# Kernel optimization log

Hardware: AMD Instinct MI355X
Metric: run time of the kernel (lower is better)

The kernel has to match this reference:

```python
import jax, jax.numpy as jnp
import numpy as np

N_NODES, N_EDGES, N_GRAPHS = 20000, 320000, 16
F_NODE, F_EDGE, F_GLOB = 64, 32, 16


def seg_mean(x, idx, num):
    # segment average; segments with zero members yield zeros
    s = jax.ops.segment_sum(x, idx, num_segments=num)
    c = jax.ops.segment_sum(jnp.ones((x.shape[0], 1), x.dtype), idx, num_segments=num)
    return s / jnp.maximum(c, 1.0)


def setup_inputs() -> dict:
    key = jax.random.key(0)
    ks = jax.random.split(key, 24)
    s = 0.05
    inp = {
        'node_feats': jax.random.normal(ks[0], (N_NODES, F_NODE), jnp.float32),
        'edge_feats': jax.random.normal(ks[1], (N_EDGES, F_EDGE), jnp.float32),
        'globals_': jax.random.normal(ks[2], (N_GRAPHS, F_GLOB), jnp.float32),
        'We1': jax.random.normal(ks[3], (256, F_EDGE), jnp.float32) * s,
        'be1': jnp.zeros((256,), jnp.float32),
        'Wn1': jax.random.normal(ks[4], (256, F_NODE), jnp.float32) * s,
        'Win1': jax.random.normal(ks[5], (256, 256), jnp.float32) * s,
        'bn1': jnp.zeros((256,), jnp.float32),
        'We2': jax.random.normal(ks[6], (128, 256), jnp.float32) * s,
        'Wg2': jax.random.normal(ks[7], (128, F_GLOB), jnp.float32) * s,
        'be2': jnp.zeros((128,), jnp.float32),
        'Wn2': jax.random.normal(ks[8], (128, 256), jnp.float32) * s,
        'Win2': jax.random.normal(ks[9], (128, 128), jnp.float32) * s,
        'Wng2': jax.random.normal(ks[10], (128, F_GLOB), jnp.float32) * s,
        'bn2': jnp.zeros((128,), jnp.float32),
        'Wgn': jax.random.normal(ks[11], (128, 128), jnp.float32) * s,
        'Wge': jax.random.normal(ks[12], (128, 128), jnp.float32) * s,
        'Wgg': jax.random.normal(ks[13], (128, F_GLOB), jnp.float32) * s,
        'bg': jnp.zeros((128,), jnp.float32),
        'receivers': jax.random.randint(ks[14], (N_EDGES,), 0, N_NODES, jnp.int32),
        'node_graph': jnp.sort(jax.random.randint(ks[15], (N_NODES,), 0, N_GRAPHS, jnp.int32)),
    }
    return inp


def reference(node_feats, edge_feats, globals_, We1, be1, Wn1, Win1, bn1,
              We2, Wg2, be2, Wn2, Win2, Wng2, bn2, Wgn, Wge, Wgg, bg,
              receivers, node_graph):
    N = node_feats.shape[0]
    B = globals_.shape[0]
    edge_graph = node_graph[receivers]  # graph id of each edge [E]

    # edge1 + relu: e -> 256
    e1 = jax.nn.relu(edge_feats @ We1.T + be1)  # [E,256]
    # node1 + relu: node + avg incoming edges -> 256
    agg1 = seg_mean(e1, receivers, N)  # [N,256]
    n1 = jax.nn.relu(node_feats @ Wn1.T + agg1 @ Win1.T + bn1)  # [N,256]
    # edge2 + relu: edge + broadcast globals -> 128
    e2 = jax.nn.relu(e1 @ We2.T + globals_[edge_graph] @ Wg2.T + be2)  # [E,128]
    # node2 + relu: node + avg incoming edges + broadcast globals -> 128
    agg2 = seg_mean(e2, receivers, N)  # [N,128]
    n2 = jax.nn.relu(n1 @ Wn2.T + agg2 @ Win2.T + globals_[node_graph] @ Wng2.T + bn2)  # [N,128]
    # global: avg nodes + avg edges per graph + globals -> output
    node_avg = seg_mean(n2, node_graph, B)  # [B,128]
    edge_avg = seg_mean(e2, edge_graph, B)  # [B,128]
    out = node_avg @ Wgn.T + edge_avg @ Wge.T + globals_ @ Wgg.T + bg  # [B,128]
    return out
```

## Files before the change

### kernel.cpp

```cpp
#include <hip/hip_runtime.h>
#include <hip/hip_bf16.h>

#define N_NODES 20000
#define N_EDGES 320000
#define NG 16

using bf16 = __hip_bfloat16;
typedef __attribute__((ext_vector_type(8))) short short8v;
typedef __attribute__((ext_vector_type(4))) short short4v;
typedef __attribute__((ext_vector_type(4))) float f32x4;

static __device__ __forceinline__ short f2bs(float f) {
  bf16 h = __float2bfloat16(f);
  union { bf16 b; short s; } u;
  u.b = h;
  return u.s;
}
static __device__ __forceinline__ float bs2f(short s) {
  union { short s; bf16 b; } u;
  u.s = s;
  return __bfloat162float(u.b);
}

__global__ __launch_bounds__(256) void k_prep(
    const float* __restrict__ globals_, const float* __restrict__ Wg2,
    const float* __restrict__ Wng2, const float* __restrict__ Wgg,
    const float* __restrict__ bg, float* __restrict__ g2e,
    float* __restrict__ g2n, float* __restrict__ gg,
    const float* __restrict__ We1, const float* __restrict__ Wn1,
    const float* __restrict__ Win1, const float* __restrict__ We2,
    const float* __restrict__ Wn2, const float* __restrict__ Win2,
    bf16* __restrict__ Wb_e1, bf16* __restrict__ Wb_n1,
    bf16* __restrict__ Wb_e2, bf16* __restrict__ Wb_n2,
    const float* __restrict__ nf, bf16* __restrict__ nfb) {
  int idx = blockIdx.x * 256 + threadIdx.x;
  if (idx < 6144) {
    int arr = idx >> 11;
    int rem = idx & 2047;
    int g = rem >> 7, c = rem & 127;
    const float* W = arr == 0 ? Wg2 : (arr == 1 ? Wng2 : Wgg);
    float acc = (arr == 2) ? bg[c] : 0.f;
#pragma unroll
    for (int k = 0; k < 16; ++k) acc += globals_[g * 16 + k] * W[c * 16 + k];
    float* o = arr == 0 ? g2e : (arr == 1 ? g2n : gg);
    o[rem] = acc;
    return;
  }
  idx -= 6144;
  if (idx < 172032) {
    int i = idx;
    float v;
    bf16* dst;
    int di;
    if (i < 8192) {
      v = We1[i]; dst = Wb_e1; di = i;
    } else if (i < 90112) {
      int j = i - 8192, r = j / 320, c = j % 320;
      v = c < 64 ? Wn1[r * 64 + c] : Win1[r * 256 + (c - 64)];
      dst = Wb_n1; di = j;
    } else if (i < 122880) {
      int j = i - 90112;
      int n = j >> 8, p = j & 255;
      int k = ((p & 15) << 4) | (p >> 4);
      v = We2[n * 256 + k];
      dst = Wb_e2; di = j;
    } else {
      int j = i - 122880, r = j / 384, c = j % 384;
      if (c < 256) {
        int k = ((c & 15) << 4) | (c >> 4);
        v = Wn2[r * 256 + k];
      } else {
        v = Win2[r * 128 + (c - 256)];
      }
      dst = Wb_n2; di = j;
    }
    dst[di] = __float2bfloat16(v);
    return;
  }
  idx -= 172032;
  if (idx < 320000) {
    int n = idx >> 4, q = idx & 15;
    float4 v = *(const float4*)(nf + (size_t)n * 64 + q * 4);
    short4v o = {f2bs(v.x), f2bs(v.y), f2bs(v.z), f2bs(v.w)};
    *(short4v*)((short*)nfb + (size_t)n * 64 + q * 4) = o;
  }
}

__global__ __launch_bounds__(256) void k_counts(
    const int* __restrict__ recv, const int* __restrict__ node_graph,
    int* __restrict__ cnt_node, int* __restrict__ node_cnt_g,
    int* __restrict__ edge_cnt_g) {
  __shared__ int le[NG], ln[NG];
  int tid = threadIdx.x;
  if (tid < NG) { le[tid] = 0; ln[tid] = 0; }
  __syncthreads();
  int idx = blockIdx.x * 256 + tid;
  if (idx < N_EDGES) {
    int r = recv[idx];
    atomicAdd(&cnt_node[r], 1);
    atomicAdd(&le[node_graph[r]], 1);
  } else if (idx < N_EDGES + N_NODES) {
    int n = idx - N_EDGES;
    atomicAdd(&ln[node_graph[n]], 1);
  }
  __syncthreads();
  if (tid < NG && le[tid]) atomicAdd(&edge_cnt_g[tid], le[tid]);
  if (tid >= NG && tid < 2 * NG && ln[tid - NG]) atomicAdd(&node_cnt_g[tid - NG], ln[tid - NG]);
}

__global__ __launch_bounds__(256) void k_scan(const int* __restrict__ cnt,
                                              int* __restrict__ offset,
                                              int* __restrict__ cursor) {
  __shared__ int wsum[4];
  __shared__ int carry_s;
  int tid = threadIdx.x, lane = tid & 63, wv = tid >> 6;
  if (tid == 0) carry_s = 0;
  __syncthreads();
  for (int base = 0; base < N_NODES; base += 1024) {
    int idx = base + tid * 4;
    int v[4];
    int s = 0;
#pragma unroll
    for (int i = 0; i < 4; ++i) {
      v[i] = (idx + i < N_NODES) ? cnt[idx + i] : 0;
      s += v[i];
    }
    int ps = s;
#pragma unroll
    for (int d = 1; d < 64; d <<= 1) {
      int t = __shfl_up(ps, d, 64);
      if (lane >= d) ps += t;
    }
    if (lane == 63) wsum[wv] = ps;
    __syncthreads();
    int wbase = carry_s;
    for (int w2 = 0; w2 < wv; ++w2) wbase += wsum[w2];
    int run = wbase + ps - s;
#pragma unroll
    for (int i = 0; i < 4; ++i) {
      if (idx + i < N_NODES) {
        offset[idx + i] = run;
        cursor[idx + i] = 0;
      }
      run += v[i];
    }
    __syncthreads();
    if (tid == 0) carry_s += wsum[0] + wsum[1] + wsum[2] + wsum[3];
    __syncthreads();
  }
  if (tid == 0) offset[N_NODES] = carry_s;
}

__global__ __launch_bounds__(256) void k_scatter(
    const int* __restrict__ recv, const int* __restrict__ offset,
    int* __restrict__ cursor, int* __restrict__ pos2edge,
    int* __restrict__ pos2node) {
  int e = blockIdx.x * 256 + threadIdx.x;
  if (e >= N_EDGES) return;
  int n = recv[e];
  int slot = atomicAdd(&cursor[n], 1);
  int pos = offset[n] + slot;
  pos2edge[pos] = e;
  pos2node[pos] = n;
}

__global__ __launch_bounds__(256, 3) void k_edge(
    const float* __restrict__ edge_feats, const bf16* __restrict__ We1b,
    const bf16* __restrict__ We2b, const float* __restrict__ be1,
    const float* __restrict__ be2, const float* __restrict__ g2e,
    const int* __restrict__ pos2edge, const int* __restrict__ pos2node,
    const int* __restrict__ node_graph, const int* __restrict__ offset,
    float* __restrict__ agg1f, float* __restrict__ agg2f) {
  __shared__ __align__(16) char wlds[16384];
  __shared__ __align__(16) short t16[64 * 264];
  __shared__ int rownode_s[64];
  __shared__ int rowgid_s[64];
  const int tid = threadIdx.x;
  const int wave = tid >> 6, lane = tid & 63;
  const int l15 = lane & 15, grp = lane >> 4;
  const int p0 = blockIdx.x * 64;
  const int base = wave * 16;

  if (tid < 64) {
    int rn = pos2node[p0 + tid];
    rownode_s[tid] = rn;
    rowgid_s[tid] = node_graph[rn];
  }
  const int n0w = tid >> 3, cgw = tid & 7;
  short8v wreg[4];
#pragma unroll
  for (int s = 0; s < 4; ++s)
    wreg[s] = *(const short8v*)((const short*)We2b + (size_t)(n0w + s * 32) * 256 + cgw * 8);
#pragma unroll
  for (int s = 0; s < 4; ++s) {
    int slot = tid + s * 256;
    int n = slot >> 2, cg = slot & 3;
    short8v w8 = *(const short8v*)((const short*)We1b + n * 32 + cg * 8);
    *(short8v*)(wlds + n * 64 + ((cg * 16) ^ (((n >> 1) & 3) << 4))) = w8;
  }
  int e = pos2edge[p0 + base + l15];
  const float* efrow = edge_feats + (size_t)e * 32 + grp * 8;
  float4 af0 = *(const float4*)(efrow);
  float4 af1 = *(const float4*)(efrow + 4);
  short8v a1;
  a1[0] = f2bs(af0.x); a1[1] = f2bs(af0.y); a1[2] = f2bs(af0.z); a1[3] = f2bs(af0.w);
  a1[4] = f2bs(af1.x); a1[5] = f2bs(af1.y); a1[6] = f2bs(af1.z); a1[7] = f2bs(af1.w);
  __syncthreads();

  f32x4 acc1[16] = {};
#pragma unroll
  for (int nf = 0; nf < 16; ++nf) {
    int n = nf * 16 + l15;
    short8v b8 = *(const short8v*)(wlds + n * 64 + ((grp * 16) ^ (((n >> 1) & 3) << 4)));
    acc1[nf] = __builtin_amdgcn_mfma_f32_16x16x32_bf16(a1, b8, acc1[nf], 0, 0, 0);
  }
#pragma unroll
  for (int nf = 0; nf < 16; ++nf) {
    float bv = be1[nf * 16 + l15];
#pragma unroll
    for (int i = 0; i < 4; ++i) {
      float v = acc1[nf][i] + bv;
      acc1[nf][i] = v > 0.f ? v : 0.f;
    }
  }
#pragma unroll
  for (int i = 0; i < 4; ++i) {
    int row = base + grp * 4 + i;
    short8v lo, hi;
#pragma unroll
    for (int q = 0; q < 8; ++q) {
      lo[q] = f2bs(acc1[q][i]);
      hi[q] = f2bs(acc1[q + 8][i]);
    }
    *(short8v*)&t16[row * 264 + l15 * 16] = lo;
    *(short8v*)&t16[row * 264 + l15 * 16 + 8] = hi;
  }
  __syncthreads();

#pragma unroll
  for (int s = 0; s < 4; ++s) {
    int n = n0w + s * 32;
    *(short8v*)(wlds + n * 128 + ((cgw * 16) ^ ((n & 7) << 4))) = wreg[s];
  }
#pragma unroll
  for (int s = 0; s < 4; ++s)
    wreg[s] = *(const short8v*)((const short*)We2b + (size_t)(n0w + s * 32) * 256 + 64 + cgw * 8);

  bool bnd = (lane == 63) || (rownode_s[lane + 1] != rownode_s[lane]);
  unsigned long long fmask = __ballot(bnd);
  unsigned long long amask = 0;
  {
    unsigned long long lsb = fmask & (~fmask + 1ull);
    if (offset[rownode_s[0]] < p0) amask |= lsb;
    if (offset[rownode_s[63] + 1] > p0 + 64) amask |= 1ull << 63;
  }

  short8v a2[8];
  const short* myrow = &t16[(base + l15) * 264];
#pragma unroll
  for (int s = 0; s < 8; ++s)
    a2[s] = *(const short8v*)(myrow + s * 32 + grp * 8);

  {
    int col = ((tid & 15) << 4) | (tid >> 4);
    float run = 0.f;
#pragma unroll
    for (int rb = 0; rb < 64; rb += 16) {
      float v[16];
#pragma unroll
      for (int i = 0; i < 16; ++i) v[i] = bs2f(t16[(rb + i) * 264 + tid]);
#pragma unroll
      for (int i = 0; i < 16; ++i) {
        run += v[i];
        int r = rb + i;
        if ((fmask >> r) & 1) {
          float* dst = &agg1f[(size_t)rownode_s[r] * 256 + col];
          if ((amask >> r) & 1) atomicAdd(dst, run);
          else *dst = run;
          run = 0.f;
        }
      }
    }
  }
  __syncthreads();

  f32x4 acc2[8] = {};
#pragma unroll
  for (int c = 0; c < 4; ++c) {
#pragma unroll
    for (int kki = 0; kki < 2; ++kki) {
#pragma unroll
      for (int nf = 0; nf < 8; ++nf) {
        int n = nf * 16 + l15;
        short8v b8 = *(const short8v*)(wlds + n * 128 +
                                       (((kki * 64) + grp * 16) ^ ((n & 7) << 4)));
        acc2[nf] = __builtin_amdgcn_mfma_f32_16x16x32_bf16(a2[c * 2 + kki], b8,
                                                           acc2[nf], 0, 0, 0);
      }
    }
    if (c < 3) {
      __syncthreads();
#pragma unroll
      for (int s = 0; s < 4; ++s) {
        int n = n0w + s * 32;
        *(short8v*)(wlds + n * 128 + ((cgw * 16) ^ ((n & 7) << 4))) = wreg[s];
      }
      if (c < 2) {
#pragma unroll
        for (int s = 0; s < 4; ++s)
          wreg[s] = *(const short8v*)((const short*)We2b +
                                      (size_t)(n0w + s * 32) * 256 + (c + 2) * 64 + cgw * 8);
      }
      __syncthreads();
    }
  }

  float* tf32 = (float*)t16;
  int gidr[4];
#pragma unroll
  for (int i = 0; i < 4; ++i) gidr[i] = rowgid_s[base + grp * 4 + i];
#pragma unroll
  for (int nf = 0; nf < 8; ++nf) {
    int col = nf * 16 + l15;
    float bv = be2[col];
#pragma unroll
    for (int i = 0; i < 4; ++i) {
      float v = acc2[nf][i] + bv + g2e[gidr[i] * 128 + col];
      acc2[nf][i] = v > 0.f ? v : 0.f;
    }
  }
#pragma unroll
  for (int i = 0; i < 4; ++i) {
    int row = base + grp * 4 + i;
    float4 lo = {acc2[0][i], acc2[1][i], acc2[2][i], acc2[3][i]};
    float4 hi = {acc2[4][i], acc2[5][i], acc2[6][i], acc2[7][i]};
    *(float4*)&tf32[row * 132 + l15 * 8] = lo;
    *(float4*)&tf32[row * 132 + l15 * 8 + 4] = hi;
  }
  __syncthreads();

  if (tid < 128) {
    int col = ((tid & 7) << 4) | (tid >> 3);
    float run = 0.f;
#pragma unroll
    for (int rb = 0; rb < 64; rb += 16) {
      float v[16];
#pragma unroll
      for (int i = 0; i < 16; ++i) v[i] = tf32[(rb + i) * 132 + tid];
#pragma unroll
      for (int i = 0; i < 16; ++i) {
        run += v[i];
        int r = rb + i;
        if ((fmask >> r) & 1) {
          float* dst = &agg2f[(size_t)rownode_s[r] * 128 + col];
          if ((amask >> r) & 1) atomicAdd(dst, run);
          else *dst = run;
          run = 0.f;
        }
      }
    }
  }
}

__global__ __launch_bounds__(256) void k_node(
    const bf16* __restrict__ nfb, const float* __restrict__ agg1f,
    const float* __restrict__ agg2f, const int* __restrict__ offset,
    const bf16* __restrict__ Wn1b, const bf16* __restrict__ Wn2b,
    const float* __restrict__ bn1, const float* __restrict__ bn2,
    const float* __restrict__ g2n, const int* __restrict__ node_graph,
    float* __restrict__ node_sum, float* __restrict__ edge_sum) {
  __shared__ __align__(16) char smem_w[32768];
  __shared__ __align__(16) short t16[64 * 264];
  __shared__ int rowgid_s[64];
  const int tid = threadIdx.x;
  const int wave = tid >> 6, lane = tid & 63;
  const int l15 = lane & 15, grp = lane >> 4;
  const int r0 = blockIdx.x * 64;
  const int base = wave * 16;
  const int n0w = tid >> 3, cgw = tid & 7;

  if (tid < 64) {
    int n = r0 + tid;
    rowgid_s[tid] = node_graph[n < N_NODES ? n : N_NODES - 1];
  }
  long arow = r0 + base + l15;
  if (arow >= N_NODES) arow = N_NODES - 1;
  int dg = offset[arow + 1] - offset[arow];
  const float inv = 1.f / (float)(dg > 1 ? dg : 1);

  short8v w1[8];
#pragma unroll
  for (int s = 0; s < 8; ++s)
    w1[s] = *(const short8v*)((const short*)Wn1b + (size_t)(n0w + s * 32) * 320 + cgw * 8);
  f32x4 acc1[16] = {};
#pragma unroll
  for (int c = 0; c < 5; ++c) {
    short8v a8[2];
#pragma unroll
    for (int kki = 0; kki < 2; ++kki) {
      int k = c * 64 + kki * 32 + grp * 8;
      if (c == 0) {
        a8[kki] = *(const short8v*)((const short*)nfb + (size_t)arow * 64 + k);
      } else {
        const float* p = agg1f + (size_t)arow * 256 + (k - 64);
        float4 f0 = *(const float4*)p;
        float4 f1 = *(const float4*)(p + 4);
        short8v t;
        t[0] = f2bs(f0.x * inv); t[1] = f2bs(f0.y * inv);
        t[2] = f2bs(f0.z * inv); t[3] = f2bs(f0.w * inv);
        t[4] = f2bs(f1.x * inv); t[5] = f2bs(f1.y * inv);
        t[6] = f2bs(f1.z * inv); t[7] = f2bs(f1.w * inv);
        a8[kki] = t;
      }
    }
#pragma unroll
    for (int s = 0; s < 8; ++s) {
      int n = n0w + s * 32;
      *(short8v*)(smem_w + n * 128 + ((cgw * 16) ^ ((n & 7) << 4))) = w1[s];
    }
    if (c < 4) {
#pragma unroll
      for (int s = 0; s < 8; ++s)
        w1[s] = *(const short8v*)((const short*)Wn1b +
                                  (size_t)(n0w + s * 32) * 320 + (c + 1) * 64 + cgw * 8);
    }
    __syncthreads();
#pragma unroll
    for (int kki = 0; kki < 2; ++kki) {
#pragma unroll
      for (int nf = 0; nf < 16; ++nf) {
        int wrow = nf * 16 + l15;
        short8v b8 = *(const short8v*)(smem_w + wrow * 128 +
                                       (((kki * 64) + grp * 16) ^ ((wrow & 7) << 4)));
        acc1[nf] = __builtin_amdgcn_mfma_f32_16x16x32_bf16(a8[kki], b8, acc1[nf], 0, 0, 0);
      }
    }
    __syncthreads();
  }

#pragma unroll
  for (int nf = 0; nf < 16; ++nf) {
    float bv = bn1[nf * 16 + l15];
#pragma unroll
    for (int i = 0; i < 4; ++i) {
      float v = acc1[nf][i] + bv;
      acc1[nf][i] = v > 0.f ? v : 0.f;
    }
  }
#pragma unroll
  for (int i = 0; i < 4; ++i) {
    int row = base + grp * 4 + i;
    short8v lo, hi;
#pragma unroll
    for (int q = 0; q < 8; ++q) {
      lo[q] = f2bs(acc1[q][i]);
      hi[q] = f2bs(acc1[q + 8][i]);
    }
    *(short8v*)&t16[row * 264 + l15 * 16] = lo;
    *(short8v*)&t16[row * 264 + l15 * 16 + 8] = hi;
  }
  short8v a2[8];
  const short* myrow = &t16[(base + l15) * 264];
#pragma unroll
  for (int s = 0; s < 8; ++s)
    a2[s] = *(const short8v*)(myrow + s * 32 + grp * 8);

  short8v w2[4];
#pragma unroll
  for (int s = 0; s < 4; ++s)
    w2[s] = *(const short8v*)((const short*)Wn2b + (size_t)(n0w + s * 32) * 384 + cgw * 8);
  f32x4 acc2[8] = {};
#pragma unroll
  for (int c = 0; c < 6; ++c) {
    short8v a8[2];
#pragma unroll
    for (int kki = 0; kki < 2; ++kki) {
      if (c < 4) {
        a8[kki] = a2[c * 2 + kki];
      } else {
        int k = (c - 4) * 64 + kki * 32 + grp * 8;
        const float* p = agg2f + (size_t)arow * 128 + k;
        float4 f0 = *(const float4*)p;
        float4 f1 = *(const float4*)(p + 4);
        short8v t;
        t[0] = f2bs(f0.x * inv); t[1] = f2bs(f0.y * inv);
        t[2] = f2bs(f0.z * inv); t[3] = f2bs(f0.w * inv);
        t[4] = f2bs(f1.x * inv); t[5] = f2bs(f1.y * inv);
        t[6] = f2bs(f1.z * inv); t[7] = f2bs(f1.w * inv);
        a8[kki] = t;
      }
    }
#pragma unroll
    for (int s = 0; s < 4; ++s) {
      int n = n0w + s * 32;
      if (n < 128)
        *(short8v*)(smem_w + n * 128 + ((cgw * 16) ^ ((n & 7) << 4))) = w2[s];
    }
    if (c < 5) {
#pragma unroll
      for (int s = 0; s < 4; ++s)
        w2[s] = *(const short8v*)((const short*)Wn2b +
                                  (size_t)(n0w + s * 32) * 384 + (c + 1) * 64 + cgw * 8);
    }
    __syncthreads();
#pragma unroll
    for (int kki = 0; kki < 2; ++kki) {
#pragma unroll
      for (int nf = 0; nf < 8; ++nf) {
        int wrow = nf * 16 + l15;
        short8v b8 = *(const short8v*)(smem_w + wrow * 128 +
                                       (((kki * 64) + grp * 16) ^ ((wrow & 7) << 4)));
        acc2[nf] = __builtin_amdgcn_mfma_f32_16x16x32_bf16(a8[kki], b8, acc2[nf], 0, 0, 0);
      }
    }
    __syncthreads();
  }

  float* tf32 = (float*)t16;
  int gidr[4];
#pragma unroll
  for (int i = 0; i < 4; ++i) gidr[i] = rowgid_s[base + grp * 4 + i];
#pragma unroll
  for (int nf = 0; nf < 8; ++nf) {
    int col = nf * 16 + l15;
    float bv = bn2[col];
#pragma unroll
    for (int i = 0; i < 4; ++i) {
      float v = acc2[nf][i] + bv + g2n[gidr[i] * 128 + col];
      acc2[nf][i] = v > 0.f ? v : 0.f;
    }
  }
#pragma unroll
  for (int i = 0; i < 4; ++i) {
    int row = base + grp * 4 + i;
    float4 lo = {acc2[0][i], acc2[1][i], acc2[2][i], acc2[3][i]};
    float4 hi = {acc2[4][i], acc2[5][i], acc2[6][i], acc2[7][i]};
    *(float4*)&tf32[row * 132 + l15 * 8] = lo;
    *(float4*)&tf32[row * 132 + l15 * 8 + 4] = hi;
  }
  __syncthreads();

  bool gb = (lane == 63) || (rowgid_s[lane + 1] != rowgid_s[lane]);
  unsigned long long gmask = __ballot(gb);
  if (tid < 128) {
    int col = ((tid & 7) << 4) | (tid >> 3);
    float rn_ = 0.f, re_ = 0.f;
#pragma unroll
    for (int rb = 0; rb < 64; rb += 16) {
      float vn[16], ve[16];
#pragma unroll
      for (int i = 0; i < 16; ++i) {
        int r = rb + i;
        long row = (long)r0 + r;
        bool ok = row < N_NODES;
        vn[i] = ok ? tf32[r * 132 + tid] : 0.f;
        ve[i] = ok ? agg2f[(size_t)row * 128 + col] : 0.f;
      }
#pragma unroll
      for (int i = 0; i < 16; ++i) {
        int r = rb + i;
        rn_ += vn[i];
        re_ += ve[i];
        if ((gmask >> r) & 1) {
          int g = rowgid_s[r];
          atomicAdd(&node_sum[g * 128 + col], rn_);
          atomicAdd(&edge_sum[g * 128 + col], re_);
          rn_ = 0.f;
          re_ = 0.f;
        }
      }
    }
  }
}

__global__ __launch_bounds__(128) void k_final(
    const float* __restrict__ node_sum, const float* __restrict__ edge_sum,
    const int* __restrict__ node_cnt_g, const int* __restrict__ edge_cnt_g,
    const float* __restrict__ Wgn, const float* __restrict__ Wge,
    const float* __restrict__ gg, float* __restrict__ out) {
  __shared__ float navg[128], eavg[128];
  const int g = blockIdx.x, c = threadIdx.x;
  int nc = node_cnt_g[g];
  nc = nc > 1 ? nc : 1;
  int ec = edge_cnt_g[g];
  ec = ec > 1 ? ec : 1;
  navg[c] = node_sum[g * 128 + c] / (float)nc;
  eavg[c] = edge_sum[g * 128 + c] / (float)ec;
  __syncthreads();
  float acc = gg[g * 128 + c];
#pragma unroll 4
  for (int k = 0; k < 128; ++k)
    acc += navg[k] * Wgn[c * 128 + k] + eavg[k] * Wge[c * 128 + k];
  out[g * 128 + c] = acc;
}

extern "C" void kernel_launch(void* const* d_in, const int* in_sizes, int n_in,
                              void* d_out, int out_size, void* d_ws, size_t ws_size,
                              hipStream_t stream) {
  const float* node_feats = (const float*)d_in[0];
  const float* edge_feats = (const float*)d_in[1];
  const float* globals_ = (const float*)d_in[2];
  const float* We1 = (const float*)d_in[3];
  const float* be1 = (const float*)d_in[4];
  const float* Wn1 = (const float*)d_in[5];
  const float* Win1 = (const float*)d_in[6];
  const float* bn1 = (const float*)d_in[7];
  const float* We2 = (const float*)d_in[8];
  const float* Wg2 = (const float*)d_in[9];
  const float* be2 = (const float*)d_in[10];
  const float* Wn2 = (const float*)d_in[11];
  const float* Win2 = (const float*)d_in[12];
  const float* Wng2 = (const float*)d_in[13];
  const float* bn2 = (const float*)d_in[14];
  const float* Wgn = (const float*)d_in[15];
  const float* Wge = (const float*)d_in[16];
  const float* Wgg = (const float*)d_in[17];
  const float* bg = (const float*)d_in[18];
  const int* receivers = (const int*)d_in[19];
  const int* node_graph = (const int*)d_in[20];
  float* out = (float*)d_out;

  char* ws = (char*)d_ws;
  size_t off = 0;
  auto alloc = [&](size_t bytes) {
    size_t o = off;
    off += (bytes + 255) & ~(size_t)255;
    return o;
  };
  const int NP = 20032;
  int* cnt_node = (int*)(ws + alloc((size_t)N_NODES * 4));
  int* node_cnt_g = (int*)(ws + alloc(NG * 4));
  int* edge_cnt_g = (int*)(ws + alloc(NG * 4));
  float* node_sum = (float*)(ws + alloc(NG * 128 * 4));
  float* edge_sum = (float*)(ws + alloc(NG * 128 * 4));
  float* agg1f = (float*)(ws + alloc((size_t)N_NODES * 256 * 4));
  float* agg2f = (float*)(ws + alloc((size_t)N_NODES * 128 * 4));
  size_t zero_bytes = off;
  int* offset = (int*)(ws + alloc((size_t)(N_NODES + 1) * 4));
  int* cursor = (int*)(ws + alloc((size_t)N_NODES * 4));
  int* pos2edge = (int*)(ws + alloc((size_t)N_EDGES * 4));
  int* pos2node = (int*)(ws + alloc((size_t)N_EDGES * 4));
  float* g2e = (float*)(ws + alloc(NG * 128 * 4));
  float* g2n = (float*)(ws + alloc(NG * 128 * 4));
  float* gg = (float*)(ws + alloc(NG * 128 * 4));
  bf16* Wb_e1 = (bf16*)(ws + alloc(8192 * 2));
  bf16* Wb_n1 = (bf16*)(ws + alloc(81920 * 2));
  bf16* Wb_e2 = (bf16*)(ws + alloc(32768 * 2));
  bf16* Wb_n2 = (bf16*)(ws + alloc(49152 * 2));
  bf16* nfb = (bf16*)(ws + alloc((size_t)NP * 64 * 2));
  (void)ws_size;

  hipMemsetAsync(d_ws, 0, zero_bytes, stream);
  k_prep<<<1946, 256, 0, stream>>>(globals_, Wg2, Wng2, Wgg, bg, g2e, g2n, gg,
                                   We1, Wn1, Win1, We2, Wn2, Win2, Wb_e1,
                                   Wb_n1, Wb_e2, Wb_n2, node_feats, nfb);
  k_counts<<<(N_EDGES + N_NODES + 255) / 256, 256, 0, stream>>>(
      receivers, node_graph, cnt_node, node_cnt_g, edge_cnt_g);
  k_scan<<<1, 256, 0, stream>>>(cnt_node, offset, cursor);
  k_scatter<<<(N_EDGES + 255) / 256, 256, 0, stream>>>(receivers, offset,
                                                       cursor, pos2edge,
                                                       pos2node);
  k_edge<<<N_EDGES / 64, 256, 0, stream>>>(edge_feats, Wb_e1, Wb_e2, be1, be2,
                                           g2e, pos2edge, pos2node, node_graph,
                                           offset, agg1f, agg2f);
  k_node<<<NP / 64, 256, 0, stream>>>(nfb, agg1f, agg2f, offset, Wb_n1, Wb_n2,
                                      bn1, bn2, g2n, node_graph, node_sum,
                                      edge_sum);
  k_final<<<NG, 128, 0, stream>>>(node_sum, edge_sum, node_cnt_g, edge_cnt_g,
                                  Wgn, Wge, gg, out);
}
```

Baseline: 205.1 us.

## Prefetch weight and activation fragments into registers ahead of MFMA loops

The edge kernel now loads all four K-chunks of We2 into registers up front instead of reloading one chunk per iteration. The node kernel preloads its full A-operand fragments (node features plus scaled aggregates) before the GEMM loops. It double-buffers Wn1 chunks two stages ahead and loads all of Wn2 into registers, with the barriers rearranged to match. This aims to hide global-load latency behind MFMA work, at the cost of much higher VGPR pressure. The launch_bounds(256,2) hint on k_node may cause spills.

```diff
diff --git a/kernel.cpp b/kernel.cpp
--- a/kernel.cpp
+++ b/kernel.cpp
@@ -187,10 +187,13 @@
     rowgid_s[tid] = node_graph[rn];
   }
   const int n0w = tid >> 3, cgw = tid & 7;
-  short8v wreg[4];
-#pragma unroll
-  for (int s = 0; s < 4; ++s)
-    wreg[s] = *(const short8v*)((const short*)We2b + (size_t)(n0w + s * 32) * 256 + cgw * 8);
+  short8v wreg[16];
+#pragma unroll
+  for (int c = 0; c < 4; ++c)
+#pragma unroll
+    for (int s = 0; s < 4; ++s)
+      wreg[c * 4 + s] = *(const short8v*)((const short*)We2b +
+                                          (size_t)(n0w + s * 32) * 256 + c * 64 + cgw * 8);
 #pragma unroll
   for (int s = 0; s < 4; ++s) {
     int slot = tid + s * 256;
@@ -242,9 +245,6 @@
     int n = n0w + s * 32;
     *(short8v*)(wlds + n * 128 + ((cgw * 16) ^ ((n & 7) << 4))) = wreg[s];
   }
-#pragma unroll
-  for (int s = 0; s < 4; ++s)
-    wreg[s] = *(const short8v*)((const short*)We2b + (size_t)(n0w + s * 32) * 256 + 64 + cgw * 8);
 
   bool bnd = (lane == 63) || (rownode_s[lane + 1] != rownode_s[lane]);
   unsigned long long fmask = __ballot(bnd);
@@ -303,13 +303,7 @@
 #pragma unroll
       for (int s = 0; s < 4; ++s) {
         int n = n0w + s * 32;
-        *(short8v*)(wlds + n * 128 + ((cgw * 16) ^ ((n & 7) << 4))) = wreg[s];
-      }
-      if (c < 2) {
-#pragma unroll
-        for (int s = 0; s < 4; ++s)
-          wreg[s] = *(const short8v*)((const short*)We2b +
-                                      (size_t)(n0w + s * 32) * 256 + (c + 2) * 64 + cgw * 8);
+        *(short8v*)(wlds + n * 128 + ((cgw * 16) ^ ((n & 7) << 4))) = wreg[(c + 1) * 4 + s];
       }
       __syncthreads();
     }
@@ -362,7 +356,7 @@
   }
 }
 
-__global__ __launch_bounds__(256) void k_node(
+__global__ __launch_bounds__(256, 2) void k_node(
     const bf16* __restrict__ nfb, const float* __restrict__ agg1f,
     const float* __restrict__ agg2f, const int* __restrict__ offset,
     const bf16* __restrict__ Wn1b, const bf16* __restrict__ Wn2b,
@@ -388,41 +382,52 @@
   int dg = offset[arow + 1] - offset[arow];
   const float inv = 1.f / (float)(dg > 1 ? dg : 1);
 
-  short8v w1[8];
-#pragma unroll
-  for (int s = 0; s < 8; ++s)
-    w1[s] = *(const short8v*)((const short*)Wn1b + (size_t)(n0w + s * 32) * 320 + cgw * 8);
-  f32x4 acc1[16] = {};
-#pragma unroll
-  for (int c = 0; c < 5; ++c) {
-    short8v a8[2];
+  short8v a1all[10];
+#pragma unroll
+  for (int kki = 0; kki < 2; ++kki)
+    a1all[kki] = *(const short8v*)((const short*)nfb + (size_t)arow * 64 + kki * 32 + grp * 8);
+#pragma unroll
+  for (int c = 1; c < 5; ++c) {
 #pragma unroll
     for (int kki = 0; kki < 2; ++kki) {
       int k = c * 64 + kki * 32 + grp * 8;
-      if (c == 0) {
-        a8[kki] = *(const short8v*)((const short*)nfb + (size_t)arow * 64 + k);
-      } else {
-        const float* p = agg1f + (size_t)arow * 256 + (k - 64);
-        float4 f0 = *(const float4*)p;
-        float4 f1 = *(const float4*)(p + 4);
-        short8v t;
-        t[0] = f2bs(f0.x * inv); t[1] = f2bs(f0.y * inv);
-        t[2] = f2bs(f0.z * inv); t[3] = f2bs(f0.w * inv);
-        t[4] = f2bs(f1.x * inv); t[5] = f2bs(f1.y * inv);
-        t[6] = f2bs(f1.z * inv); t[7] = f2bs(f1.w * inv);
-        a8[kki] = t;
-      }
-    }
+      const float* p = agg1f + (size_t)arow * 256 + (k - 64);
+      float4 f0 = *(const float4*)p;
+      float4 f1 = *(const float4*)(p + 4);
+      short8v t;
+      t[0] = f2bs(f0.x * inv); t[1] = f2bs(f0.y * inv);
+      t[2] = f2bs(f0.z * inv); t[3] = f2bs(f0.w * inv);
+      t[4] = f2bs(f1.x * inv); t[5] = f2bs(f1.y * inv);
+      t[6] = f2bs(f1.z * inv); t[7] = f2bs(f1.w * inv);
+      a1all[c * 2 + kki] = t;
+    }
+  }
+
+  short8v w1x[8], w1y[8];
+#pragma unroll
+  for (int s = 0; s < 8; ++s)
+    w1x[s] = *(const short8v*)((const short*)Wn1b + (size_t)(n0w + s * 32) * 320 + cgw * 8);
+#pragma unroll
+  for (int s = 0; s < 8; ++s)
+    w1y[s] = *(const short8v*)((const short*)Wn1b + (size_t)(n0w + s * 32) * 320 + 64 + cgw * 8);
+  f32x4 acc1[16] = {};
+#pragma unroll
+  for (int c = 0; c < 5; ++c) {
+    if (c > 0) __syncthreads();
 #pragma unroll
     for (int s = 0; s < 8; ++s) {
       int n = n0w + s * 32;
-      *(short8v*)(smem_w + n * 128 + ((cgw * 16) ^ ((n & 7) << 4))) = w1[s];
-    }
-    if (c < 4) {
-#pragma unroll
-      for (int s = 0; s < 8; ++s)
-        w1[s] = *(const short8v*)((const short*)Wn1b +
-                                  (size_t)(n0w + s * 32) * 320 + (c + 1) * 64 + cgw * 8);
+      *(short8v*)(smem_w + n * 128 + ((cgw * 16) ^ ((n & 7) << 4))) =
+          (c & 1) ? w1y[s] : w1x[s];
+    }
+    if (c + 2 < 5) {
+#pragma unroll
+      for (int s = 0; s < 8; ++s) {
+        short8v t = *(const short8v*)((const short*)Wn1b +
+                                      (size_t)(n0w + s * 32) * 320 + (c + 2) * 64 + cgw * 8);
+        if (c & 1) w1y[s] = t;
+        else w1x[s] = t;
+      }
     }
     __syncthreads();
 #pragma unroll
@@ -432,10 +437,10 @@
         int wrow = nf * 16 + l15;
         short8v b8 = *(const short8v*)(smem_w + wrow * 128 +
                                        (((kki * 64) + grp * 16) ^ ((wrow & 7) << 4)));
-        acc1[nf] = __builtin_amdgcn_mfma_f32_16x16x32_bf16(a8[kki], b8, acc1[nf], 0, 0, 0);
-      }
-    }
-    __syncthreads();
+        acc1[nf] = __builtin_amdgcn_mfma_f32_16x16x32_bf16(a1all[c * 2 + kki], b8,
+                                                           acc1[nf], 0, 0, 0);
+      }
+    }
   }
 
 #pragma unroll
@@ -459,48 +464,43 @@
     *(short8v*)&t16[row * 264 + l15 * 16] = lo;
     *(short8v*)&t16[row * 264 + l15 * 16 + 8] = hi;
   }
-  short8v a2[8];
+  short8v a2all[12];
   const short* myrow = &t16[(base + l15) * 264];
 #pragma unroll
   for (int s = 0; s < 8; ++s)
-    a2[s] = *(const short8v*)(myrow + s * 32 + grp * 8);
-
-  short8v w2[4];
-#pragma unroll
-  for (int s = 0; s < 4; ++s)
-    w2[s] = *(const short8v*)((const short*)Wn2b + (size_t)(n0w + s * 32) * 384 + cgw * 8);
+    a2all[s] = *(const short8v*)(myrow + s * 32 + grp * 8);
+#pragma unroll
+  for (int c = 4; c < 6; ++c) {
+#pragma unroll
+    for (int kki = 0; kki < 2; ++kki) {
+      int k = (c - 4) * 64 + kki * 32 + grp * 8;
+      const float* p = agg2f + (size_t)arow * 128 + k;
+      float4 f0 = *(const float4*)p;
+      float4 f1 = *(const float4*)(p + 4);
+      short8v t;
+      t[0] = f2bs(f0.x * inv); t[1] = f2bs(f0.y * inv);
+      t[2] = f2bs(f0.z * inv); t[3] = f2bs(f0.w * inv);
+      t[4] = f2bs(f1.x * inv); t[5] = f2bs(f1.y * inv);
+      t[6] = f2bs(f1.z * inv); t[7] = f2bs(f1.w * inv);
+      a2all[c * 2 + kki] = t;
+    }
+  }
+  short8v w2r[24];
+#pragma unroll
+  for (int c = 0; c < 6; ++c)
+#pragma unroll
+    for (int s = 0; s < 4; ++s)
+      w2r[c * 4 + s] = *(const short8v*)((const short*)Wn2b +
+                                         (size_t)(n0w + s * 32) * 384 + c * 64 + cgw * 8);
+
   f32x4 acc2[8] = {};
 #pragma unroll
   for (int c = 0; c < 6; ++c) {
-    short8v a8[2];
-#pragma unroll
-    for (int kki = 0; kki < 2; ++kki) {
-      if (c < 4) {
-        a8[kki] = a2[c * 2 + kki];
-      } else {
-        int k = (c - 4) * 64 + kki * 32 + grp * 8;
-        const float* p = agg2f + (size_t)arow * 128 + k;
-        float4 f0 = *(const float4*)p;
-        float4 f1 = *(const float4*)(p + 4);
-        short8v t;
-        t[0] = f2bs(f0.x * inv); t[1] = f2bs(f0.y * inv);
-        t[2] = f2bs(f0.z * inv); t[3] = f2bs(f0.w * inv);
-        t[4] = f2bs(f1.x * inv); t[5] = f2bs(f1.y * inv);
-        t[6] = f2bs(f1.z * inv); t[7] = f2bs(f1.w * inv);
-        a8[kki] = t;
-      }
-    }
+    __syncthreads();
 #pragma unroll
     for (int s = 0; s < 4; ++s) {
       int n = n0w + s * 32;
-      if (n < 128)
-        *(short8v*)(smem_w + n * 128 + ((cgw * 16) ^ ((n & 7) << 4))) = w2[s];
-    }
-    if (c < 5) {
-#pragma unroll
-      for (int s = 0; s < 4; ++s)
-        w2[s] = *(const short8v*)((const short*)Wn2b +
-                                  (size_t)(n0w + s * 32) * 384 + (c + 1) * 64 + cgw * 8);
+      *(short8v*)(smem_w + n * 128 + ((cgw * 16) ^ ((n & 7) << 4))) = w2r[c * 4 + s];
     }
     __syncthreads();
 #pragma unroll
@@ -510,10 +510,10 @@
         int wrow = nf * 16 + l15;
         short8v b8 = *(const short8v*)(smem_w + wrow * 128 +
                                        (((kki * 64) + grp * 16) ^ ((wrow & 7) << 4)));
-        acc2[nf] = __builtin_amdgcn_mfma_f32_16x16x32_bf16(a8[kki], b8, acc2[nf], 0, 0, 0);
-      }
-    }
-    __syncthreads();
+        acc2[nf] = __builtin_amdgcn_mfma_f32_16x16x32_bf16(a2all[c * 2 + kki], b8,
+                                                           acc2[nf], 0, 0, 0);
+      }
+    }
   }
 
   float* tf32 = (float*)t16;
```

New measurement: 201.5 us. About the same (-1.7%).
